# Kernel tuning notes

Hardware: AMD Instinct MI355X
Metric: run time of the kernel (lower is better)

## Reference

```python
import jax, jax.numpy as jnp
import numpy as np

SEQ, BS, H, I, E = 2048, 4, 2048, 4096, 8


def setup_inputs() -> dict:
    key = jax.random.key(0)
    ks = jax.random.split(key, 5)
    s = 0.02
    return {
        "hidden_states": jax.random.normal(ks[0], (SEQ, BS, H), dtype=jnp.float32),
        "router_w": jax.random.normal(ks[1], (H, E), dtype=jnp.float32) * s,
        "gate_w": jax.random.normal(ks[2], (E, H, I), dtype=jnp.float32) * s,
        "up_w": jax.random.normal(ks[3], (E, H, I), dtype=jnp.float32) * s,
        "down_w": jax.random.normal(ks[4], (E, I, H), dtype=jnp.float32) * s,
    }


def reference(hidden_states, router_w, gate_w, up_w, down_w):
    # Router: [S,B,H] @ [H,E] -> [S,B,E]; top-1 routing (num_experts_per_tok == 1)
    router_logits = jnp.einsum("sbh,he->sbe", hidden_states, router_w)
    routing_indices = jnp.argmax(router_logits, axis=-1)  # [S,B]
    # sigmoid routing weights are computed but NOT applied in the original combine
    routing_weights = jax.nn.sigmoid(jnp.max(router_logits, axis=-1))  # noqa: F841

    out = jnp.zeros_like(hidden_states)
    for e in range(E):  # small fixed expert count
        mask = (routing_indices == e)[..., None]  # [S,B,1]
        g = jnp.einsum("sbh,hi->sbi", hidden_states, gate_w[e])
        u = jnp.einsum("sbh,hi->sbi", hidden_states, up_w[e])
        y = jnp.einsum("sbi,ih->sbh", jax.nn.silu(g) * u, down_w[e])
        out = out + jnp.where(mask, y, jnp.zeros((), out.dtype))
    return out
```

## Files before the change

kernel.cpp:

```cpp
#include <hip/hip_runtime.h>
#include <hip/hip_bf16.h>

#define T_TOKENS 8192
#define H_DIM 2048
#define I_DIM 4096
#define E_EXP 8
#define PAD_ROWS 9216

typedef __bf16 bf16x8 __attribute__((ext_vector_type(8)));
typedef float floatx4 __attribute__((ext_vector_type(4)));
typedef unsigned short ushort8 __attribute__((ext_vector_type(8)));

__device__ __forceinline__ unsigned short f2bf(float f) {
  union { float f; unsigned int i; } c; c.f = f;
  unsigned int x = c.i;
  unsigned int r = x + 0x7fffu + ((x >> 16) & 1u);
  return (unsigned short)(r >> 16);
}

__device__ __forceinline__ float bf2float(unsigned short u) {
  union { unsigned int i; float f; } c; c.i = ((unsigned int)u) << 16;
  return c.f;
}

__device__ __forceinline__ void gload_lds16(const void* g, void* l) {
  __builtin_amdgcn_global_load_lds(
      (const __attribute__((address_space(1))) void*)g,
      (__attribute__((address_space(3))) void*)l, 16, 0, 0);
}

__global__ __launch_bounds__(256) void xcvt_kernel(const float* __restrict__ x,
                                                   unsigned short* __restrict__ xb,
                                                   int* __restrict__ hdr) {
  if (blockIdx.x == 0 && threadIdx.x < 32) hdr[threadIdx.x] = 0;
  int i = (blockIdx.x * 256 + threadIdx.x) * 4;
  floatx4 v = *(const floatx4*)(x + i);
  unsigned short o0 = f2bf(v[0]), o1 = f2bf(v[1]), o2 = f2bf(v[2]), o3 = f2bf(v[3]);
  ushort4 o; o.x = o0; o.y = o1; o.z = o2; o.w = o3;
  *(ushort4*)(xb + i) = o;
}

__global__ __launch_bounds__(256) void router_kernel(const float* __restrict__ x,
                                                     const float* __restrict__ rw,
                                                     int* __restrict__ idx,
                                                     int* __restrict__ hdr) {
  int lane = threadIdx.x & 63;
  int t = blockIdx.x * 4 + (threadIdx.x >> 6);
  const float* xr = x + (size_t)t * H_DIM;
  float acc[8];
#pragma unroll
  for (int e = 0; e < 8; ++e) acc[e] = 0.f;
  for (int i = lane; i < H_DIM; i += 64) {
    float h = xr[i];
    floatx4 r0 = *(const floatx4*)(rw + i * 8);
    floatx4 r1 = *(const floatx4*)(rw + i * 8 + 4);
#pragma unroll
    for (int e = 0; e < 4; ++e) { acc[e] += h * r0[e]; acc[e + 4] += h * r1[e]; }
  }
#pragma unroll
  for (int off = 32; off > 0; off >>= 1)
#pragma unroll
    for (int e = 0; e < 8; ++e) acc[e] += __shfl_xor(acc[e], off, 64);
  if (lane == 0) {
    int best = 0; float bv = acc[0];
#pragma unroll
    for (int e = 1; e < 8; ++e) if (acc[e] > bv) { bv = acc[e]; best = e; }
    idx[t] = best;
    atomicAdd(&hdr[best], 1);
  }
}

__global__ __launch_bounds__(256) void setup_kernel(int* __restrict__ hdr,
                                                    int* __restrict__ rows) {
  if (threadIdx.x == 0) {
    int b = 0;
    for (int e = 0; e < 8; ++e) {
      hdr[16 + e] = b;
      b += ((hdr[e] + 127) >> 7) << 7;
    }
  }
  for (int i = threadIdx.x; i < PAD_ROWS; i += 256) rows[i] = -1;
}

__global__ __launch_bounds__(256) void scatter_kernel(const int* __restrict__ idx,
                                                      int* __restrict__ hdr,
                                                      int* __restrict__ rows) {
  int t = blockIdx.x * 256 + threadIdx.x;
  int e = idx[t];
  int p = atomicAdd(&hdr[8 + e], 1);
  rows[hdr[16 + e] + p] = t;
}

template <int K, int N>
__global__ __launch_bounds__(256) void wtrans_kernel(const float* __restrict__ W,
                                                     unsigned short* __restrict__ Wt) {
  __shared__ unsigned short tile[64 * 64];
  const int e = blockIdx.z;
  const int bn = blockIdx.x * 64;
  const int bk = blockIdx.y * 64;
  const float* Wp = W + (size_t)e * K * N + (size_t)bk * N + bn;
  unsigned short* Wtp = Wt + (size_t)e * N * K + (size_t)bn * K + bk;
  const int tid = threadIdx.x;

  {
    const int kq = tid >> 4;
    const int nq = tid & 15;
    floatx4 v[4];
#pragma unroll
    for (int i = 0; i < 4; ++i)
      v[i] = *(const floatx4*)(Wp + (size_t)(kq * 4 + i) * N + nq * 4);
    const int s16 = kq >> 1;
    const int half = kq & 1;
#pragma unroll
    for (int j = 0; j < 4; ++j) {
      const int n = nq * 4 + j;
      ushort4 t;
      t.x = f2bf(v[0][j]); t.y = f2bf(v[1][j]);
      t.z = f2bf(v[2][j]); t.w = f2bf(v[3][j]);
      *(ushort4*)(tile + n * 64 + ((s16 ^ (n & 7)) << 3) + half * 4) = t;
    }
  }
  __syncthreads();
  {
    const int kc = tid & 7;
    const int nr = tid >> 3;
#pragma unroll
    for (int it = 0; it < 2; ++it) {
      const int n = it * 32 + nr;
      ushort8 o = *(const ushort8*)(tile + n * 64 + ((kc ^ (n & 7)) << 3));
      *(ushort8*)(Wtp + (size_t)n * K + kc * 8) = o;
    }
  }
}

__global__ __launch_bounds__(256, 2) void moe_gemm_gu(
    const unsigned short* __restrict__ A,
    const unsigned short* __restrict__ Bg,
    const unsigned short* __restrict__ Bu,
    const int* __restrict__ hdr,
    const int* __restrict__ rows,
    unsigned short* __restrict__ inter) {
  const int e = blockIdx.z;
  const int cnt = hdr[e];
  if ((int)blockIdx.y * 128 >= cnt) return;
  const int seg = hdr[16 + e];

  const int tid = threadIdx.x;
  const int lane = tid & 63;
  const int wv = tid >> 6;
  const int wm = (wv & 1) * 64;
  const int wn = (wv >> 1) * 64;
  const int q = lane >> 4;
  const int l15 = lane & 15;

  __shared__ unsigned short sA[128 * 64];
  __shared__ unsigned short sBg[128 * 64];
  __shared__ unsigned short sBu[128 * 64];

  const int lr = lane >> 3;
  const int colsw = (lane & 7) ^ lr;
  const unsigned short* aptr[4];
  const unsigned short* bgptr[4];
  const unsigned short* buptr[4];
  const unsigned short* BgE = Bg + (size_t)e * I_DIM * H_DIM;
  const unsigned short* BuE = Bu + (size_t)e * I_DIM * H_DIM;
#pragma unroll
  for (int j = 0; j < 4; ++j) {
    const int R = j * 32 + wv * 8 + lr;
    int ar = rows[seg + blockIdx.y * 128 + R];
    if (ar < 0) ar = 0;
    aptr[j] = A + (size_t)ar * H_DIM + colsw * 8;
    bgptr[j] = BgE + (size_t)(blockIdx.x * 128 + R) * H_DIM + colsw * 8;
    buptr[j] = BuE + (size_t)(blockIdx.x * 128 + R) * H_DIM + colsw * 8;
  }

  floatx4 accg[4][4], accu[4][4];
#pragma unroll
  for (int a = 0; a < 4; ++a)
#pragma unroll
    for (int b = 0; b < 4; ++b) {
      accg[a][b] = (floatx4){0.f, 0.f, 0.f, 0.f};
      accu[a][b] = (floatx4){0.f, 0.f, 0.f, 0.f};
    }

  for (int kt = 0; kt < H_DIM; kt += 64) {
#pragma unroll
    for (int j = 0; j < 4; ++j) {
      gload_lds16(aptr[j] + kt, sA + (j * 32 + wv * 8) * 64);
      gload_lds16(bgptr[j] + kt, sBg + (j * 32 + wv * 8) * 64);
      gload_lds16(buptr[j] + kt, sBu + (j * 32 + wv * 8) * 64);
    }
    __syncthreads();
#pragma unroll
    for (int ks = 0; ks < 64; ks += 32) {
      const int sbase = ks >> 3;
      bf16x8 af[4], bfr[4];
#pragma unroll
      for (int fm = 0; fm < 4; ++fm) {
        const int ra = wm + fm * 16 + l15;
        af[fm] = __builtin_bit_cast(bf16x8,
            *(const ushort8*)(sA + ra * 64 + (((q + sbase) ^ (ra & 7)) << 3)));
      }
#pragma unroll
      for (int fn = 0; fn < 4; ++fn) {
        const int rb = wn + fn * 16 + l15;
        bfr[fn] = __builtin_bit_cast(bf16x8,
            *(const ushort8*)(sBg + rb * 64 + (((q + sbase) ^ (rb & 7)) << 3)));
      }
#pragma unroll
      for (int fm = 0; fm < 4; ++fm)
#pragma unroll
        for (int fn = 0; fn < 4; ++fn)
          accg[fm][fn] = __builtin_amdgcn_mfma_f32_16x16x32_bf16(af[fm], bfr[fn],
                                                                 accg[fm][fn], 0, 0, 0);
#pragma unroll
      for (int fn = 0; fn < 4; ++fn) {
        const int rb = wn + fn * 16 + l15;
        bfr[fn] = __builtin_bit_cast(bf16x8,
            *(const ushort8*)(sBu + rb * 64 + (((q + sbase) ^ (rb & 7)) << 3)));
      }
#pragma unroll
      for (int fm = 0; fm < 4; ++fm)
#pragma unroll
        for (int fn = 0; fn < 4; ++fn)
          accu[fm][fn] = __builtin_amdgcn_mfma_f32_16x16x32_bf16(af[fm], bfr[fn],
                                                                 accu[fm][fn], 0, 0, 0);
    }
    __syncthreads();
  }

#pragma unroll
  for (int fm = 0; fm < 4; ++fm)
#pragma unroll
    for (int fn = 0; fn < 4; ++fn)
#pragma unroll
      for (int rr = 0; rr < 4; ++rr) {
        const int row = wm + fm * 16 + q * 4 + rr;
        const int col = wn + fn * 16 + l15;
        const int gm = blockIdx.y * 128 + row;
        const int gn = blockIdx.x * 128 + col;
        const float g = accg[fm][fn][rr];
        const float u = accu[fm][fn][rr];
        const float s = g / (1.f + __expf(-g));
        inter[(size_t)(seg + gm) * I_DIM + gn] = f2bf(s * u);
      }
}

__global__ __launch_bounds__(256, 2) void moe_gemm_down(
    const unsigned short* __restrict__ A,
    const unsigned short* __restrict__ Bt,
    const int* __restrict__ hdr,
    const int* __restrict__ rows,
    float* __restrict__ outp) {
  const int e = blockIdx.z;
  const int cnt = hdr[e];
  if ((int)blockIdx.y * 128 >= cnt) return;
  const int seg = hdr[16 + e];

  const int tid = threadIdx.x;
  const int lane = tid & 63;
  const int wv = tid >> 6;
  const int wm = (wv & 1) * 64;
  const int wn = (wv >> 1) * 64;
  const int q = lane >> 4;
  const int l15 = lane & 15;

  __shared__ unsigned short sA[128 * 64];
  __shared__ unsigned short sB0[128 * 64];
  __shared__ unsigned short sB1[128 * 64];

  const int lr = lane >> 3;
  const int colsw = (lane & 7) ^ lr;
  const unsigned short* aptr[4];
  const unsigned short* b0ptr[4];
  const unsigned short* b1ptr[4];
  const unsigned short* Be = Bt + (size_t)e * H_DIM * I_DIM;
#pragma unroll
  for (int j = 0; j < 4; ++j) {
    const int R = j * 32 + wv * 8 + lr;
    aptr[j]  = A + (size_t)(seg + blockIdx.y * 128 + R) * I_DIM + colsw * 8;
    b0ptr[j] = Be + (size_t)(blockIdx.x * 256 + R) * I_DIM + colsw * 8;
    b1ptr[j] = Be + (size_t)(blockIdx.x * 256 + 128 + R) * I_DIM + colsw * 8;
  }

  floatx4 acc0[4][4], acc1[4][4];
#pragma unroll
  for (int a = 0; a < 4; ++a)
#pragma unroll
    for (int b = 0; b < 4; ++b) {
      acc0[a][b] = (floatx4){0.f, 0.f, 0.f, 0.f};
      acc1[a][b] = (floatx4){0.f, 0.f, 0.f, 0.f};
    }

  for (int kt = 0; kt < I_DIM; kt += 64) {
#pragma unroll
    for (int j = 0; j < 4; ++j) {
      gload_lds16(aptr[j] + kt, sA + (j * 32 + wv * 8) * 64);
      gload_lds16(b0ptr[j] + kt, sB0 + (j * 32 + wv * 8) * 64);
      gload_lds16(b1ptr[j] + kt, sB1 + (j * 32 + wv * 8) * 64);
    }
    __syncthreads();
#pragma unroll
    for (int ks = 0; ks < 64; ks += 32) {
      const int sbase = ks >> 3;
      bf16x8 af[4], bfr[4];
#pragma unroll
      for (int fm = 0; fm < 4; ++fm) {
        const int ra = wm + fm * 16 + l15;
        af[fm] = __builtin_bit_cast(bf16x8,
            *(const ushort8*)(sA + ra * 64 + (((q + sbase) ^ (ra & 7)) << 3)));
      }
#pragma unroll
      for (int fn = 0; fn < 4; ++fn) {
        const int rb = wn + fn * 16 + l15;
        bfr[fn] = __builtin_bit_cast(bf16x8,
            *(const ushort8*)(sB0 + rb * 64 + (((q + sbase) ^ (rb & 7)) << 3)));
      }
#pragma unroll
      for (int fm = 0; fm < 4; ++fm)
#pragma unroll
        for (int fn = 0; fn < 4; ++fn)
          acc0[fm][fn] = __builtin_amdgcn_mfma_f32_16x16x32_bf16(af[fm], bfr[fn],
                                                                 acc0[fm][fn], 0, 0, 0);
#pragma unroll
      for (int fn = 0; fn < 4; ++fn) {
        const int rb = wn + fn * 16 + l15;
        bfr[fn] = __builtin_bit_cast(bf16x8,
            *(const ushort8*)(sB1 + rb * 64 + (((q + sbase) ^ (rb & 7)) << 3)));
      }
#pragma unroll
      for (int fm = 0; fm < 4; ++fm)
#pragma unroll
        for (int fn = 0; fn < 4; ++fn)
          acc1[fm][fn] = __builtin_amdgcn_mfma_f32_16x16x32_bf16(af[fm], bfr[fn],
                                                                 acc1[fm][fn], 0, 0, 0);
    }
    __syncthreads();
  }

#pragma unroll
  for (int fm = 0; fm < 4; ++fm)
#pragma unroll
    for (int rr = 0; rr < 4; ++rr) {
      const int row = wm + fm * 16 + q * 4 + rr;
      const int tok = rows[seg + blockIdx.y * 128 + row];
      if (tok < 0) continue;
      float* orow = outp + (size_t)tok * H_DIM + blockIdx.x * 256;
#pragma unroll
      for (int fn = 0; fn < 4; ++fn) {
        const int col = wn + fn * 16 + l15;
        orow[col]       = acc0[fm][fn][rr];
        orow[128 + col] = acc1[fm][fn][rr];
      }
    }
}

extern "C" void kernel_launch(void* const* d_in, const int* in_sizes, int n_in,
                              void* d_out, int out_size, void* d_ws, size_t ws_size,
                              hipStream_t stream) {
  const float* hidden   = (const float*)d_in[0];
  const float* router_w = (const float*)d_in[1];
  const float* gate_w   = (const float*)d_in[2];
  const float* up_w     = (const float*)d_in[3];
  const float* down_w   = (const float*)d_in[4];
  float* out = (float*)d_out;

  char* ws = (char*)d_ws;
  int* hdr  = (int*)ws;
  int* idx  = (int*)(ws + 1024);
  int* rows = (int*)(ws + 33792);
  unsigned short* x_bf  = (unsigned short*)(ws + 70656);
  unsigned short* inter = (unsigned short*)(ws + 33625088);
  unsigned short* W1    = (unsigned short*)(ws + 109122560);
  unsigned short* W2    = (unsigned short*)(ws + 243340288);
  unsigned short* downt = W1;

  xcvt_kernel<<<T_TOKENS * H_DIM / 1024, 256, 0, stream>>>(hidden, x_bf, hdr);
  router_kernel<<<T_TOKENS / 4, 256, 0, stream>>>(hidden, router_w, idx, hdr);
  setup_kernel<<<1, 256, 0, stream>>>(hdr, rows);
  scatter_kernel<<<T_TOKENS / 256, 256, 0, stream>>>(idx, hdr, rows);

  wtrans_kernel<H_DIM, I_DIM><<<dim3(I_DIM / 64, H_DIM / 64, E_EXP), 256, 0, stream>>>(gate_w, W1);
  wtrans_kernel<H_DIM, I_DIM><<<dim3(I_DIM / 64, H_DIM / 64, E_EXP), 256, 0, stream>>>(up_w, W2);

  moe_gemm_gu<<<dim3(I_DIM / 128, 64, E_EXP), 256, 0, stream>>>(
      x_bf, W1, W2, hdr, rows, inter);

  wtrans_kernel<I_DIM, H_DIM><<<dim3(H_DIM / 64, I_DIM / 64, E_EXP), 256, 0, stream>>>(down_w, downt);
  moe_gemm_down<<<dim3(H_DIM / 256, 64, E_EXP), 256, 0, stream>>>(
      inter, downt, hdr, rows, out);
}
```

Measured before the change: 1.504 ms.

## Replace weight transpose with MFMA-fragment-tiled bf16 layout for direct LDS loads

The weight conversion no longer transposes through shared memory. It now writes bf16 weights in blocks of 8 k by 16 n, so each 16-byte chunk already matches an MFMA B fragment. Both GEMMs load these blocks straight into LDS and read B fragments without XOR swizzle address math. This removes the shared-memory transpose and its barrier from the conversion kernels, and simplifies B addressing in the GEMMs. The risk is LDS bank conflicts on the unswizzled B reads and less coalesced global reads in the conversion kernel.

Result: no change. 1.497 ms (-0.4%).

```diff
diff --git a/kernel.cpp b/kernel.cpp
--- a/kernel.cpp
+++ b/kernel.cpp
@@ -92,44 +92,25 @@
 }
 
 template <int K, int N>
-__global__ __launch_bounds__(256) void wtrans_kernel(const float* __restrict__ W,
-                                                     unsigned short* __restrict__ Wt) {
-  __shared__ unsigned short tile[64 * 64];
+__global__ __launch_bounds__(256) void cvt_tile_kernel(const float* __restrict__ W,
+                                                       unsigned short* __restrict__ Wt) {
   const int e = blockIdx.z;
-  const int bn = blockIdx.x * 64;
-  const int bk = blockIdx.y * 64;
-  const float* Wp = W + (size_t)e * K * N + (size_t)bk * N + bn;
-  unsigned short* Wtp = Wt + (size_t)e * N * K + (size_t)bn * K + bk;
+  const int kg = blockIdx.y;
+  const int nb = blockIdx.x * 1024;
+  const float* src = W + (size_t)e * K * N + (size_t)kg * 8 * N + nb;
+  unsigned short* dst = Wt + (size_t)e * K * N
+                        + ((size_t)kg * (N / 16) + (nb >> 4)) * 128;
   const int tid = threadIdx.x;
-
-  {
-    const int kq = tid >> 4;
-    const int nq = tid & 15;
-    floatx4 v[4];
-#pragma unroll
-    for (int i = 0; i < 4; ++i)
-      v[i] = *(const floatx4*)(Wp + (size_t)(kq * 4 + i) * N + nq * 4);
-    const int s16 = kq >> 1;
-    const int half = kq & 1;
-#pragma unroll
-    for (int j = 0; j < 4; ++j) {
-      const int n = nq * 4 + j;
-      ushort4 t;
-      t.x = f2bf(v[0][j]); t.y = f2bf(v[1][j]);
-      t.z = f2bf(v[2][j]); t.w = f2bf(v[3][j]);
-      *(ushort4*)(tile + n * 64 + ((s16 ^ (n & 7)) << 3) + half * 4) = t;
-    }
-  }
-  __syncthreads();
-  {
-    const int kc = tid & 7;
-    const int nr = tid >> 3;
-#pragma unroll
-    for (int it = 0; it < 2; ++it) {
-      const int n = it * 32 + nr;
-      ushort8 o = *(const ushort8*)(tile + n * 64 + ((kc ^ (n & 7)) << 3));
-      *(ushort8*)(Wtp + (size_t)n * K + kc * 8) = o;
-    }
+#pragma unroll
+  for (int j = 0; j < 4; ++j) {
+    const int n = j * 256 + tid;
+    float v[8];
+#pragma unroll
+    for (int kk = 0; kk < 8; ++kk) v[kk] = src[(size_t)kk * N + n];
+    ushort8 o;
+#pragma unroll
+    for (int kk = 0; kk < 8; ++kk) o[kk] = f2bf(v[kk]);
+    *(ushort8*)(dst + (size_t)(n >> 4) * 128 + (n & 15) * 8) = o;
   }
 }
 
@@ -154,25 +135,24 @@
   const int l15 = lane & 15;
 
   __shared__ unsigned short sA[128 * 64];
-  __shared__ unsigned short sBg[128 * 64];
-  __shared__ unsigned short sBu[128 * 64];
+  __shared__ unsigned short sBg[64 * 128];
+  __shared__ unsigned short sBu[64 * 128];
 
   const int lr = lane >> 3;
   const int colsw = (lane & 7) ^ lr;
   const unsigned short* aptr[4];
-  const unsigned short* bgptr[4];
-  const unsigned short* buptr[4];
-  const unsigned short* BgE = Bg + (size_t)e * I_DIM * H_DIM;
-  const unsigned short* BuE = Bu + (size_t)e * I_DIM * H_DIM;
 #pragma unroll
   for (int j = 0; j < 4; ++j) {
     const int R = j * 32 + wv * 8 + lr;
     int ar = rows[seg + blockIdx.y * 128 + R];
     if (ar < 0) ar = 0;
     aptr[j] = A + (size_t)ar * H_DIM + colsw * 8;
-    bgptr[j] = BgE + (size_t)(blockIdx.x * 128 + R) * H_DIM + colsw * 8;
-    buptr[j] = BuE + (size_t)(blockIdx.x * 128 + R) * H_DIM + colsw * 8;
-  }
+  }
+
+  const int N16 = I_DIM / 16;
+  const int ng0 = blockIdx.x * 8;
+  const unsigned short* BgE = Bg + (size_t)e * I_DIM * H_DIM;
+  const unsigned short* BuE = Bu + (size_t)e * I_DIM * H_DIM;
 
   floatx4 accg[4][4], accu[4][4];
 #pragma unroll
@@ -183,17 +163,24 @@
       accu[a][b] = (floatx4){0.f, 0.f, 0.f, 0.f};
     }
 
+  const int ubB = q * 1024 + l15 * 8;
+  const int wn16o = (wn >> 4) * 128;
+
   for (int kt = 0; kt < H_DIM; kt += 64) {
 #pragma unroll
     for (int j = 0; j < 4; ++j) {
       gload_lds16(aptr[j] + kt, sA + (j * 32 + wv * 8) * 64);
-      gload_lds16(bgptr[j] + kt, sBg + (j * 32 + wv * 8) * 64);
-      gload_lds16(buptr[j] + kt, sBu + (j * 32 + wv * 8) * 64);
+      const int g = j * 4 + wv;
+      const int kgg = (kt >> 3) + (g >> 1);
+      const size_t so = (size_t)(kgg * N16 + ng0 + (g & 1) * 4) * 128 + lane * 8;
+      gload_lds16(BgE + so, sBg + g * 512);
+      gload_lds16(BuE + so, sBu + g * 512);
     }
     __syncthreads();
 #pragma unroll
     for (int ks = 0; ks < 64; ks += 32) {
       const int sbase = ks >> 3;
+      const int bbase = ks * 128 + wn16o + ubB;
       bf16x8 af[4], bfr[4];
 #pragma unroll
       for (int fm = 0; fm < 4; ++fm) {
@@ -202,11 +189,9 @@
             *(const ushort8*)(sA + ra * 64 + (((q + sbase) ^ (ra & 7)) << 3)));
       }
 #pragma unroll
-      for (int fn = 0; fn < 4; ++fn) {
-        const int rb = wn + fn * 16 + l15;
+      for (int fn = 0; fn < 4; ++fn)
         bfr[fn] = __builtin_bit_cast(bf16x8,
-            *(const ushort8*)(sBg + rb * 64 + (((q + sbase) ^ (rb & 7)) << 3)));
-      }
+            *(const ushort8*)(sBg + bbase + fn * 128));
 #pragma unroll
       for (int fm = 0; fm < 4; ++fm)
 #pragma unroll
@@ -214,11 +199,9 @@
           accg[fm][fn] = __builtin_amdgcn_mfma_f32_16x16x32_bf16(af[fm], bfr[fn],
                                                                  accg[fm][fn], 0, 0, 0);
 #pragma unroll
-      for (int fn = 0; fn < 4; ++fn) {
-        const int rb = wn + fn * 16 + l15;
+      for (int fn = 0; fn < 4; ++fn)
         bfr[fn] = __builtin_bit_cast(bf16x8,
-            *(const ushort8*)(sBu + rb * 64 + (((q + sbase) ^ (rb & 7)) << 3)));
-      }
+            *(const ushort8*)(sBu + bbase + fn * 128));
 #pragma unroll
       for (int fm = 0; fm < 4; ++fm)
 #pragma unroll
@@ -266,22 +249,21 @@
   const int l15 = lane & 15;
 
   __shared__ unsigned short sA[128 * 64];
-  __shared__ unsigned short sB0[128 * 64];
-  __shared__ unsigned short sB1[128 * 64];
+  __shared__ unsigned short sB0[64 * 128];
+  __shared__ unsigned short sB1[64 * 128];
 
   const int lr = lane >> 3;
   const int colsw = (lane & 7) ^ lr;
   const unsigned short* aptr[4];
-  const unsigned short* b0ptr[4];
-  const unsigned short* b1ptr[4];
-  const unsigned short* Be = Bt + (size_t)e * H_DIM * I_DIM;
 #pragma unroll
   for (int j = 0; j < 4; ++j) {
     const int R = j * 32 + wv * 8 + lr;
-    aptr[j]  = A + (size_t)(seg + blockIdx.y * 128 + R) * I_DIM + colsw * 8;
-    b0ptr[j] = Be + (size_t)(blockIdx.x * 256 + R) * I_DIM + colsw * 8;
-    b1ptr[j] = Be + (size_t)(blockIdx.x * 256 + 128 + R) * I_DIM + colsw * 8;
-  }
+    aptr[j] = A + (size_t)(seg + blockIdx.y * 128 + R) * I_DIM + colsw * 8;
+  }
+
+  const int N16 = H_DIM / 16;
+  const int ng0 = blockIdx.x * 16;
+  const unsigned short* Be = Bt + (size_t)e * H_DIM * I_DIM;
 
   floatx4 acc0[4][4], acc1[4][4];
 #pragma unroll
@@ -292,17 +274,25 @@
       acc1[a][b] = (floatx4){0.f, 0.f, 0.f, 0.f};
     }
 
+  const int ubB = q * 1024 + l15 * 8;
+  const int wn16o = (wn >> 4) * 128;
+
   for (int kt = 0; kt < I_DIM; kt += 64) {
 #pragma unroll
     for (int j = 0; j < 4; ++j) {
       gload_lds16(aptr[j] + kt, sA + (j * 32 + wv * 8) * 64);
-      gload_lds16(b0ptr[j] + kt, sB0 + (j * 32 + wv * 8) * 64);
-      gload_lds16(b1ptr[j] + kt, sB1 + (j * 32 + wv * 8) * 64);
+      const int g = j * 4 + wv;
+      const int kgg = (kt >> 3) + (g >> 1);
+      const size_t so0 = (size_t)(kgg * N16 + ng0 + (g & 1) * 4) * 128 + lane * 8;
+      const size_t so1 = (size_t)(kgg * N16 + ng0 + 8 + (g & 1) * 4) * 128 + lane * 8;
+      gload_lds16(Be + so0, sB0 + g * 512);
+      gload_lds16(Be + so1, sB1 + g * 512);
     }
     __syncthreads();
 #pragma unroll
     for (int ks = 0; ks < 64; ks += 32) {
       const int sbase = ks >> 3;
+      const int bbase = ks * 128 + wn16o + ubB;
       bf16x8 af[4], bfr[4];
 #pragma unroll
       for (int fm = 0; fm < 4; ++fm) {
@@ -311,11 +301,9 @@
             *(const ushort8*)(sA + ra * 64 + (((q + sbase) ^ (ra & 7)) << 3)));
       }
 #pragma unroll
-      for (int fn = 0; fn < 4; ++fn) {
-        const int rb = wn + fn * 16 + l15;
+      for (int fn = 0; fn < 4; ++fn)
         bfr[fn] = __builtin_bit_cast(bf16x8,
-            *(const ushort8*)(sB0 + rb * 64 + (((q + sbase) ^ (rb & 7)) << 3)));
-      }
+            *(const ushort8*)(sB0 + bbase + fn * 128));
 #pragma unroll
       for (int fm = 0; fm < 4; ++fm)
 #pragma unroll
@@ -323,11 +311,9 @@
           acc0[fm][fn] = __builtin_amdgcn_mfma_f32_16x16x32_bf16(af[fm], bfr[fn],
                                                                  acc0[fm][fn], 0, 0, 0);
 #pragma unroll
-      for (int fn = 0; fn < 4; ++fn) {
-        const int rb = wn + fn * 16 + l15;
+      for (int fn = 0; fn < 4; ++fn)
         bfr[fn] = __builtin_bit_cast(bf16x8,
-            *(const ushort8*)(sB1 + rb * 64 + (((q + sbase) ^ (rb & 7)) << 3)));
-      }
+            *(const ushort8*)(sB1 + bbase + fn * 128));
 #pragma unroll
       for (int fm = 0; fm < 4; ++fm)
 #pragma unroll
@@ -380,13 +366,13 @@
   setup_kernel<<<1, 256, 0, stream>>>(hdr, rows);
   scatter_kernel<<<T_TOKENS / 256, 256, 0, stream>>>(idx, hdr, rows);
 
-  wtrans_kernel<H_DIM, I_DIM><<<dim3(I_DIM / 64, H_DIM / 64, E_EXP), 256, 0, stream>>>(gate_w, W1);
-  wtrans_kernel<H_DIM, I_DIM><<<dim3(I_DIM / 64, H_DIM / 64, E_EXP), 256, 0, stream>>>(up_w, W2);
+  cvt_tile_kernel<H_DIM, I_DIM><<<dim3(I_DIM / 1024, H_DIM / 8, E_EXP), 256, 0, stream>>>(gate_w, W1);
+  cvt_tile_kernel<H_DIM, I_DIM><<<dim3(I_DIM / 1024, H_DIM / 8, E_EXP), 256, 0, stream>>>(up_w, W2);
 
   moe_gemm_gu<<<dim3(I_DIM / 128, 64, E_EXP), 256, 0, stream>>>(
       x_bf, W1, W2, hdr, rows, inter);
 
-  wtrans_kernel<I_DIM, H_DIM><<<dim3(H_DIM / 64, I_DIM / 64, E_EXP), 256, 0, stream>>>(down_w, downt);
+  cvt_tile_kernel<I_DIM, H_DIM><<<dim3(H_DIM / 1024, I_DIM / 8, E_EXP), 256, 0, stream>>>(down_w, downt);
   moe_gemm_down<<<dim3(H_DIM / 256, 64, E_EXP), 256, 0, stream>>>(
       inter, downt, hdr, rows, out);
 }
```
